# Kernel tuning notes

Hardware: AMD Instinct MI355X
Metric: run time of the kernel (lower is better)

## Reference

```python
import jax, jax.numpy as jnp
import numpy as np

C = 64        # number of classes (rows of mu)
K = 64        # int(d * overlap_ratio) = int(128 * 0.5)
ALPHA = 1.0   # margin


def _pairdist(mu, x):
    # Euclidean distance from every center to every sample: [C, N]
    d2 = (mu * mu).sum(-1)[:, None] + (x * x).sum(-1)[None, :] - 2.0 * (mu @ x.T)
    return jnp.sqrt(jnp.maximum(d2, 0.0))


def setup_inputs() -> dict:
    key = jax.random.key(0)
    k1, k2, k3 = jax.random.split(key, 3)
    N, D = 131072, 256
    x = jax.random.normal(k1, (N, D), dtype=jnp.float32)
    y = jax.random.randint(k2, (N, 3), 0, C)
    # ensure every class 0..C-1 is present with ~equal counts (matches torch.unique)
    y = y.at[:, 2].set(jnp.arange(N) % C)
    mu = jax.random.normal(k3, (C, D), dtype=jnp.float32)
    return {"x": x, "y": y, "mu": mu}


def reference(x, y, mu):
    labels = y[:, 2]                                     # [N]
    D = _pairdist(mu, x)                                 # [C, N]
    mask = labels[None, :] == jnp.arange(C)[:, None]     # [C, N] class membership

    # pos: per class c, K LARGEST distances from center c to its own samples
    pos_vals = jax.lax.top_k(jnp.where(mask, D, -jnp.inf), K)[0]  # [C, K]
    pos_mean = pos_vals.mean(-1)                                  # [C]

    # neg: for each sample-class c2, K SMALLEST distances from every center c1
    def neg_for_class(m):  # m: [N] bool mask for class c2
        vals = jax.lax.top_k(jnp.where(m[None, :], -D, -jnp.inf), K)[0]  # [C, K]
        return (-vals).mean(-1)  # [C] smallest-K mean per center c1

    negM = jax.lax.map(neg_for_class, mask)              # [C2, C1]

    hinge = jnp.maximum(ALPHA + pos_mean[None, :] - negM, 0.0)  # [C2, C1]
    offdiag = 1.0 - jnp.eye(C, dtype=hinge.dtype)
    loss = (hinge * offdiag).sum() / x.shape[0]
    return loss
```

## Files before the change

### kernel.cpp

```cpp
#include <hip/hip_runtime.h>
#include <math.h>


#define DDIM 256
#define CC 64
#define KSEL 64
#define TPTS 256
#define XS 48
#define SELN 2048

typedef short s4v __attribute__((ext_vector_type(4)));
typedef short s8v __attribute__((ext_vector_type(8)));
typedef float f4v __attribute__((ext_vector_type(4)));

__device__ __forceinline__ void cvt_split(float f, short& h, short& l) {
  const unsigned int u = __float_as_uint(f);
  const unsigned int hb = (u + 0x7FFFu + ((u >> 16) & 1u)) >> 16;
  h = (short)hb;
  const float rem = f - __uint_as_float(hb << 16);
  const unsigned int ur = __float_as_uint(rem);
  l = (short)((ur + 0x7FFFu + ((ur >> 16) & 1u)) >> 16);
}

__global__ __launch_bounds__(128) void zeroK(int* cnts) {
  cnts[threadIdx.x] = 0;
}

__global__ __launch_bounds__(256) void countK(const int* __restrict__ y, int* cnt, int N) {
  int i = blockIdx.x * 256 + threadIdx.x;
  if (i < N) atomicAdd(&cnt[y[3 * i + 2] & (CC - 1)], 1);
}

__global__ void scanK(const int* __restrict__ cnt, int* base) {
  if (threadIdx.x == 0) {
    int s = 0;
    for (int i = 0; i < CC; ++i) { base[i] = s; s += cnt[i]; }
  }
}

__global__ __launch_bounds__(256) void fillK(const int* __restrict__ y, const int* __restrict__ base,
                                             int* cnt2, int* idxs, int N) {
  int i = blockIdx.x * 256 + threadIdx.x;
  if (i < N) {
    int m = y[3 * i + 2] & (CC - 1);
    int r = atomicAdd(&cnt2[m], 1);
    idxs[base[m] + r] = i;
  }
}

__global__ __launch_bounds__(256) void distK(const float* __restrict__ x, const float* __restrict__ mu,
                                             const int* __restrict__ idxs, float* __restrict__ Dg, int N) {
  __shared__ __align__(16) short xh[TPTS][XS];
  __shared__ __align__(16) short xl[TPTS][XS];
  __shared__ __align__(16) short mh[CC][XS];
  __shared__ __align__(16) short ml[CC][XS];
  __shared__ int pid[TPTS];
  __shared__ float xn2[TPTS];
  __shared__ float mn2[CC];

  const int t = threadIdx.x;
  const int wgp0 = blockIdx.x * TPTS;
  pid[t] = idxs[wgp0 + t];

  const int q = t & 7,  pr = t >> 3;
  const int q2 = t & 3, mm = t >> 2;
  const int w = t >> 6, l = t & 63;
  const int lr = l & 15, lk = l >> 4;

  f4v acc[4][4];
  #pragma unroll
  for (int a = 0; a < 4; ++a)
    #pragma unroll
    for (int b = 0; b < 4; ++b) acc[a][b] = (f4v)0.f;
  float xnacc[8] = {0.f, 0.f, 0.f, 0.f, 0.f, 0.f, 0.f, 0.f};
  float mnacc = 0.f;

  __syncthreads();
  int pidr[8];
  #pragma unroll
  for (int r = 0; r < 8; ++r) pidr[r] = pid[r * 32 + pr];

  for (int ch = 0; ch < 8; ++ch) {
    const int kb = ch * 32;
    if (ch) __syncthreads();
    #pragma unroll
    for (int r = 0; r < 8; ++r) {
      const float4 v = *reinterpret_cast<const float4*>(x + (size_t)pidr[r] * DDIM + kb + q * 4);
      const float vs[4] = {v.x, v.y, v.z, v.w};
      s4v hv, lv;
      float s2 = 0.f;
      #pragma unroll
      for (int j = 0; j < 4; ++j) {
        short hj, lj; cvt_split(vs[j], hj, lj);
        hv[j] = hj; lv[j] = lj;
        s2 = fmaf(vs[j], vs[j], s2);
      }
      xnacc[r] += s2;
      const int p = r * 32 + pr;
      *reinterpret_cast<s4v*>(&xh[p][q * 4]) = hv;
      *reinterpret_cast<s4v*>(&xl[p][q * 4]) = lv;
    }
    {
      const float* msrc = mu + (size_t)mm * DDIM + kb + q2 * 8;
      const float4 va = *reinterpret_cast<const float4*>(msrc);
      const float4 vb = *reinterpret_cast<const float4*>(msrc + 4);
      const float vs[8] = {va.x, va.y, va.z, va.w, vb.x, vb.y, vb.z, vb.w};
      s4v h0, h1, l0, l1;
      #pragma unroll
      for (int j = 0; j < 4; ++j) {
        short hj, lj; cvt_split(vs[j], hj, lj);
        h0[j] = hj; l0[j] = lj;
        mnacc = fmaf(vs[j], vs[j], mnacc);
      }
      #pragma unroll
      for (int j = 0; j < 4; ++j) {
        short hj, lj; cvt_split(vs[4 + j], hj, lj);
        h1[j] = hj; l1[j] = lj;
        mnacc = fmaf(vs[4 + j], vs[4 + j], mnacc);
      }
      *reinterpret_cast<s4v*>(&mh[mm][q2 * 8])     = h0;
      *reinterpret_cast<s4v*>(&mh[mm][q2 * 8 + 4]) = h1;
      *reinterpret_cast<s4v*>(&ml[mm][q2 * 8])     = l0;
      *reinterpret_cast<s4v*>(&ml[mm][q2 * 8 + 4]) = l1;
    }
    __syncthreads();
    s8v ah[4], al_[4];
    #pragma unroll
    for (int mt = 0; mt < 4; ++mt) {
      ah[mt]  = *reinterpret_cast<const s8v*>(&mh[mt * 16 + lr][lk * 8]);
      al_[mt] = *reinterpret_cast<const s8v*>(&ml[mt * 16 + lr][lk * 8]);
    }
    #pragma unroll
    for (int nt = 0; nt < 4; ++nt) {
      const int prow = w * 64 + nt * 16 + lr;
      const s8v bh = *reinterpret_cast<const s8v*>(&xh[prow][lk * 8]);
      const s8v bl = *reinterpret_cast<const s8v*>(&xl[prow][lk * 8]);
      #pragma unroll
      for (int mt = 0; mt < 4; ++mt) {
        acc[mt][nt] = __builtin_amdgcn_mfma_f32_16x16x32_bf16(ah[mt],  bh, acc[mt][nt], 0, 0, 0);
        acc[mt][nt] = __builtin_amdgcn_mfma_f32_16x16x32_bf16(ah[mt],  bl, acc[mt][nt], 0, 0, 0);
        acc[mt][nt] = __builtin_amdgcn_mfma_f32_16x16x32_bf16(al_[mt], bh, acc[mt][nt], 0, 0, 0);
      }
    }
  }
  #pragma unroll
  for (int r = 0; r < 8; ++r) {
    float s = xnacc[r];
    s += __shfl_xor(s, 1, 64); s += __shfl_xor(s, 2, 64); s += __shfl_xor(s, 4, 64);
    if (q == 0) xn2[r * 32 + pr] = s;
  }
  {
    float s = mnacc;
    s += __shfl_xor(s, 1, 64); s += __shfl_xor(s, 2, 64);
    if (q2 == 0) mn2[mm] = s;
  }
  __syncthreads();
  #pragma unroll
  for (int mt = 0; mt < 4; ++mt) {
    #pragma unroll
    for (int r = 0; r < 4; ++r) {
      const int m = mt * 16 + lk * 4 + r;
      const float mn = mn2[m];
      #pragma unroll
      for (int nt = 0; nt < 4; ++nt) {
        const int p = w * 64 + nt * 16 + lr;
        const float d2 = mn + xn2[p] - 2.f * acc[mt][nt][r];
        Dg[(size_t)m * N + wgp0 + p] = sqrtf(fmaxf(d2, 0.f));
      }
    }
  }
}

__global__ __launch_bounds__(128) void selK(const float* __restrict__ Dg, const int* __restrict__ cnt,
                                            const int* __restrict__ base, float* __restrict__ posM,
                                            float* __restrict__ neg, int N) {
  __shared__ __align__(16) unsigned int keys[SELN];
  __shared__ unsigned int sh_lo, sh_hi;
  __shared__ int sh_cnt[2];
  __shared__ float sh_sum[2];
  const int c = blockIdx.x, m = blockIdx.y;
  const int t = threadIdx.x;
  const int w = t >> 6, lane = t & 63;
  const bool diag = (c == m);
  int cm = cnt[m]; if (cm > SELN) cm = SELN;
  const int bm = base[m];
  const float* src = Dg + (size_t)c * N + bm;
  const int cm4 = (cm + 3) & ~3;

  unsigned int kmin = 0xFFFFFFFFu, kmax = 0u;
  for (int i = t; i < cm4; i += 128) {
    unsigned int key = 0xFFFFFFFFu;
    if (i < cm) {
      const unsigned int b = __float_as_uint(src[i]);
      key = diag ? ~b : b;
      kmin = min(kmin, key); kmax = max(kmax, key);
    }
    keys[i] = key;
  }
  #pragma unroll
  for (int off = 32; off > 0; off >>= 1) {
    kmin = min(kmin, (unsigned int)__shfl_xor((int)kmin, off, 64));
    kmax = max(kmax, (unsigned int)__shfl_xor((int)kmax, off, 64));
  }
  if (lane == 0) { sh_cnt[w] = (int)kmin; sh_sum[w] = __uint_as_float(kmax); }
  __syncthreads();
  if (t == 0) {
    sh_lo = min((unsigned int)sh_cnt[0], (unsigned int)sh_cnt[1]);
    sh_hi = max(__float_as_uint(sh_sum[0]), __float_as_uint(sh_sum[1]));
  }

  for (;;) {
    __syncthreads();
    const unsigned int lo = sh_lo, hi = sh_hi;
    if (lo >= hi) break;
    const unsigned int mid = lo + ((hi - lo) >> 1);
    int cl = 0;
    for (int i4 = t * 4; i4 < cm4; i4 += 512) {
      const uint4 kv = *reinterpret_cast<const uint4*>(&keys[i4]);
      cl += (int)(kv.x <= mid) + (int)(kv.y <= mid) + (int)(kv.z <= mid) + (int)(kv.w <= mid);
    }
    #pragma unroll
    for (int off = 32; off > 0; off >>= 1) cl += __shfl_xor(cl, off, 64);
    if (lane == 0) sh_cnt[w] = cl;
    __syncthreads();
    if (t == 0) {
      if (sh_cnt[0] + sh_cnt[1] >= KSEL) sh_hi = mid; else sh_lo = mid + 1;
    }
  }
  const unsigned int kth = sh_lo;

  int cl = 0; float sl = 0.f;
  for (int i4 = t * 4; i4 < cm4; i4 += 512) {
    const uint4 kv = *reinterpret_cast<const uint4*>(&keys[i4]);
    const unsigned int ks[4] = {kv.x, kv.y, kv.z, kv.w};
    #pragma unroll
    for (int j = 0; j < 4; ++j) {
      if (ks[j] < kth) { ++cl; sl += __uint_as_float(diag ? ~ks[j] : ks[j]); }
    }
  }
  #pragma unroll
  for (int off = 32; off > 0; off >>= 1) {
    cl += __shfl_xor(cl, off, 64);
    sl += __shfl_xor(sl, off, 64);
  }
  if (lane == 0) { sh_cnt[w] = cl; sh_sum[w] = sl; }
  __syncthreads();
  if (t == 0) {
    const int totc = sh_cnt[0] + sh_cnt[1];
    const float tots = sh_sum[0] + sh_sum[1];
    const float kval = __uint_as_float(diag ? ~kth : kth);
    const float mval = (tots + (float)(KSEL - totc) * kval) * (1.0f / KSEL);
    if (diag) posM[c] = mval; else neg[m * CC + c] = mval;
  }
}

__global__ __launch_bounds__(256) void lossK(const float* __restrict__ posM, const float* __restrict__ neg,
                                             float* __restrict__ out, int N) {
  __shared__ float red[256];
  const int t = threadIdx.x;
  float s = 0.f;
  for (int idx = t; idx < CC * CC; idx += 256) {
    const int m = idx >> 6, c = idx & 63;
    if (m != c) {
      const float h = 1.0f + posM[c] - neg[idx];
      s += fmaxf(h, 0.0f);
    }
  }
  red[t] = s;
  __syncthreads();
  for (int off = 128; off > 0; off >>= 1) {
    if (t < off) red[t] += red[t + off];
    __syncthreads();
  }
  if (t == 0) out[0] = red[0] / (float)N;
}

__global__ void wsFailK(float* out) {
  if (threadIdx.x == 0) out[0] = -1.0e30f;
}

extern "C" void kernel_launch(void* const* d_in, const int* in_sizes, int n_in,
                              void* d_out, int out_size, void* d_ws, size_t ws_size,
                              hipStream_t stream) {
  const float* x  = (const float*)d_in[0];
  const int*   y  = (const int*)d_in[1];
  const float* mu = (const float*)d_in[2];
  float* out = (float*)d_out;
  const int N = in_sizes[0] / DDIM;

  const size_t need = (size_t)557056 + (size_t)CC * (size_t)N * 4;
  if (ws_size < need) {
    hipLaunchKernelGGL(wsFailK, dim3(1), dim3(64), 0, stream, out);
    return;
  }
  char* w = (char*)d_ws;
  int*   cnt  = (int*)(w);
  int*   cnt2 = (int*)(w + 256);
  int*   base = (int*)(w + 512);
  float* posM = (float*)(w + 768);
  float* neg  = (float*)(w + 1024);
  int*   idxs = (int*)(w + 32768);
  float* Dg   = (float*)(w + 557056);

  hipLaunchKernelGGL(zeroK, dim3(1), dim3(128), 0, stream, cnt);
  hipLaunchKernelGGL(countK, dim3((N + 255) / 256), dim3(256), 0, stream, y, cnt, N);
  hipLaunchKernelGGL(scanK, dim3(1), dim3(64), 0, stream, cnt, base);
  hipLaunchKernelGGL(fillK, dim3((N + 255) / 256), dim3(256), 0, stream, y, base, cnt2, idxs, N);
  hipLaunchKernelGGL(distK, dim3(N / TPTS), dim3(256), 0, stream, x, mu, idxs, Dg, N);
  hipLaunchKernelGGL(selK, dim3(CC, CC), dim3(128), 0, stream, Dg, cnt, base, posM, neg, N);
  hipLaunchKernelGGL(lossK, dim3(1), dim3(256), 0, stream, posM, neg, out, N);
}
```

Measured before the change: 331.6 us.

## Precompute split-bf16 mu once and prefetch x chunks in distance kernel

The zero-count kernel becomes a prep kernel that converts mu to bf16 hi/lo parts and its squared norms once, stored in the workspace. The distance kernel then reads these mu fragments straight from global memory instead of redoing the conversion and LDS staging in every block. It also halves the points per block, with launch bounds raised for more occupancy, and register-prefetches the next x chunk while the MFMAs run. The costs are more blocks, each re-reading mu fragments from global or L2, and a second barrier per chunk.

```diff
diff --git a/kernel.cpp b/kernel.cpp
--- a/kernel.cpp
+++ b/kernel.cpp
@@ -5,8 +5,8 @@
 #define DDIM 256
 #define CC 64
 #define KSEL 64
-#define TPTS 256
-#define XS 48
+#define TPTS 128
+#define XS 40
 #define SELN 2048
 
 typedef short s4v __attribute__((ext_vector_type(4)));
@@ -22,8 +22,27 @@
   l = (short)((ur + 0x7FFFu + ((ur >> 16) & 1u)) >> 16);
 }
 
-__global__ __launch_bounds__(128) void zeroK(int* cnts) {
-  cnts[threadIdx.x] = 0;
+__global__ __launch_bounds__(256) void prepK(const float* __restrict__ mu, short* __restrict__ mhG,
+                                             short* __restrict__ mlG, float* __restrict__ mn2G,
+                                             int* __restrict__ cnts) {
+  const int b = blockIdx.x, t = threadIdx.x;
+  if (b == 0 && t < 128) cnts[t] = 0;
+  const int row = b * 4 + (t >> 6), l = t & 63;
+  const float4 v = *reinterpret_cast<const float4*>(mu + (size_t)row * DDIM + l * 4);
+  const float vs[4] = {v.x, v.y, v.z, v.w};
+  s4v hv, lv;
+  float s2 = 0.f;
+  #pragma unroll
+  for (int j = 0; j < 4; ++j) {
+    short hj, lj; cvt_split(vs[j], hj, lj);
+    hv[j] = hj; lv[j] = lj;
+    s2 = fmaf(vs[j], vs[j], s2);
+  }
+  *reinterpret_cast<s4v*>(&mhG[(size_t)row * DDIM + l * 4]) = hv;
+  *reinterpret_cast<s4v*>(&mlG[(size_t)row * DDIM + l * 4]) = lv;
+  #pragma unroll
+  for (int off = 32; off > 0; off >>= 1) s2 += __shfl_xor(s2, off, 64);
+  if (l == 0) mn2G[row] = s2;
 }
 
 __global__ __launch_bounds__(256) void countK(const int* __restrict__ y, int* cnt, int N) {
@@ -48,45 +67,51 @@
   }
 }
 
-__global__ __launch_bounds__(256) void distK(const float* __restrict__ x, const float* __restrict__ mu,
-                                             const int* __restrict__ idxs, float* __restrict__ Dg, int N) {
+__global__ __launch_bounds__(256, 4) void distK(const float* __restrict__ x, const short* __restrict__ mhG,
+                                                const short* __restrict__ mlG, const float* __restrict__ mn2G,
+                                                const int* __restrict__ idxs, float* __restrict__ Dg, int N) {
   __shared__ __align__(16) short xh[TPTS][XS];
   __shared__ __align__(16) short xl[TPTS][XS];
-  __shared__ __align__(16) short mh[CC][XS];
-  __shared__ __align__(16) short ml[CC][XS];
   __shared__ int pid[TPTS];
   __shared__ float xn2[TPTS];
-  __shared__ float mn2[CC];
 
   const int t = threadIdx.x;
   const int wgp0 = blockIdx.x * TPTS;
-  pid[t] = idxs[wgp0 + t];
-
-  const int q = t & 7,  pr = t >> 3;
-  const int q2 = t & 3, mm = t >> 2;
+  if (t < TPTS) pid[t] = idxs[wgp0 + t];
+
+  const int q = t & 7, pr = t >> 3;
   const int w = t >> 6, l = t & 63;
   const int lr = l & 15, lk = l >> 4;
 
-  f4v acc[4][4];
+  f4v acc[4][2];
   #pragma unroll
   for (int a = 0; a < 4; ++a)
     #pragma unroll
-    for (int b = 0; b < 4; ++b) acc[a][b] = (f4v)0.f;
-  float xnacc[8] = {0.f, 0.f, 0.f, 0.f, 0.f, 0.f, 0.f, 0.f};
-  float mnacc = 0.f;
-
-  __syncthreads();
-  int pidr[8];
-  #pragma unroll
-  for (int r = 0; r < 8; ++r) pidr[r] = pid[r * 32 + pr];
+    for (int b = 0; b < 2; ++b) acc[a][b] = (f4v)0.f;
+  float xnacc[4] = {0.f, 0.f, 0.f, 0.f};
+
+  __syncthreads();
+  int pidr[4];
+  #pragma unroll
+  for (int p = 0; p < 4; ++p) pidr[p] = pid[p * 32 + pr];
+
+  float4 vreg[4];
+  #pragma unroll
+  for (int p = 0; p < 4; ++p)
+    vreg[p] = *reinterpret_cast<const float4*>(x + (size_t)pidr[p] * DDIM + q * 4);
 
   for (int ch = 0; ch < 8; ++ch) {
     const int kb = ch * 32;
-    if (ch) __syncthreads();
-    #pragma unroll
-    for (int r = 0; r < 8; ++r) {
-      const float4 v = *reinterpret_cast<const float4*>(x + (size_t)pidr[r] * DDIM + kb + q * 4);
-      const float vs[4] = {v.x, v.y, v.z, v.w};
+    s8v ah[4], al_[4];
+    #pragma unroll
+    for (int mt = 0; mt < 4; ++mt) {
+      const size_t ro = (size_t)(mt * 16 + lr) * DDIM + kb + lk * 8;
+      ah[mt]  = *reinterpret_cast<const s8v*>(mhG + ro);
+      al_[mt] = *reinterpret_cast<const s8v*>(mlG + ro);
+    }
+    #pragma unroll
+    for (int p = 0; p < 4; ++p) {
+      const float vs[4] = {vreg[p].x, vreg[p].y, vreg[p].z, vreg[p].w};
       s4v hv, lv;
       float s2 = 0.f;
       #pragma unroll
@@ -95,64 +120,40 @@
         hv[j] = hj; lv[j] = lj;
         s2 = fmaf(vs[j], vs[j], s2);
       }
-      xnacc[r] += s2;
-      const int p = r * 32 + pr;
-      *reinterpret_cast<s4v*>(&xh[p][q * 4]) = hv;
-      *reinterpret_cast<s4v*>(&xl[p][q * 4]) = lv;
-    }
-    {
-      const float* msrc = mu + (size_t)mm * DDIM + kb + q2 * 8;
-      const float4 va = *reinterpret_cast<const float4*>(msrc);
-      const float4 vb = *reinterpret_cast<const float4*>(msrc + 4);
-      const float vs[8] = {va.x, va.y, va.z, va.w, vb.x, vb.y, vb.z, vb.w};
-      s4v h0, h1, l0, l1;
+      xnacc[p] += s2;
+      const int pt = p * 32 + pr;
+      *reinterpret_cast<s4v*>(&xh[pt][q * 4]) = hv;
+      *reinterpret_cast<s4v*>(&xl[pt][q * 4]) = lv;
+    }
+    __syncthreads();
+    if (ch < 7) {
       #pragma unroll
-      for (int j = 0; j < 4; ++j) {
-        short hj, lj; cvt_split(vs[j], hj, lj);
-        h0[j] = hj; l0[j] = lj;
-        mnacc = fmaf(vs[j], vs[j], mnacc);
+      for (int p = 0; p < 4; ++p)
+        vreg[p] = *reinterpret_cast<const float4*>(x + (size_t)pidr[p] * DDIM + kb + 32 + q * 4);
+    }
+    s8v bh[2], bl[2];
+    #pragma unroll
+    for (int nt = 0; nt < 2; ++nt) {
+      const int prow = w * 32 + nt * 16 + lr;
+      bh[nt] = *reinterpret_cast<const s8v*>(&xh[prow][lk * 8]);
+      bl[nt] = *reinterpret_cast<const s8v*>(&xl[prow][lk * 8]);
+    }
+    #pragma unroll
+    for (int mt = 0; mt < 4; ++mt) {
+      #pragma unroll
+      for (int nt = 0; nt < 2; ++nt) {
+        acc[mt][nt] = __builtin_amdgcn_mfma_f32_16x16x32_bf16(ah[mt],  bh[nt], acc[mt][nt], 0, 0, 0);
+        acc[mt][nt] = __builtin_amdgcn_mfma_f32_16x16x32_bf16(ah[mt],  bl[nt], acc[mt][nt], 0, 0, 0);
+        acc[mt][nt] = __builtin_amdgcn_mfma_f32_16x16x32_bf16(al_[mt], bh[nt], acc[mt][nt], 0, 0, 0);
       }
-      #pragma unroll
-      for (int j = 0; j < 4; ++j) {
-        short hj, lj; cvt_split(vs[4 + j], hj, lj);
-        h1[j] = hj; l1[j] = lj;
-        mnacc = fmaf(vs[4 + j], vs[4 + j], mnacc);
-      }
-      *reinterpret_cast<s4v*>(&mh[mm][q2 * 8])     = h0;
-      *reinterpret_cast<s4v*>(&mh[mm][q2 * 8 + 4]) = h1;
-      *reinterpret_cast<s4v*>(&ml[mm][q2 * 8])     = l0;
-      *reinterpret_cast<s4v*>(&ml[mm][q2 * 8 + 4]) = l1;
-    }
-    __syncthreads();
-    s8v ah[4], al_[4];
-    #pragma unroll
-    for (int mt = 0; mt < 4; ++mt) {
-      ah[mt]  = *reinterpret_cast<const s8v*>(&mh[mt * 16 + lr][lk * 8]);
-      al_[mt] = *reinterpret_cast<const s8v*>(&ml[mt * 16 + lr][lk * 8]);
-    }
-    #pragma unroll
-    for (int nt = 0; nt < 4; ++nt) {
-      const int prow = w * 64 + nt * 16 + lr;
-      const s8v bh = *reinterpret_cast<const s8v*>(&xh[prow][lk * 8]);
-      const s8v bl = *reinterpret_cast<const s8v*>(&xl[prow][lk * 8]);
-      #pragma unroll
-      for (int mt = 0; mt < 4; ++mt) {
-        acc[mt][nt] = __builtin_amdgcn_mfma_f32_16x16x32_bf16(ah[mt],  bh, acc[mt][nt], 0, 0, 0);
-        acc[mt][nt] = __builtin_amdgcn_mfma_f32_16x16x32_bf16(ah[mt],  bl, acc[mt][nt], 0, 0, 0);
-        acc[mt][nt] = __builtin_amdgcn_mfma_f32_16x16x32_bf16(al_[mt], bh, acc[mt][nt], 0, 0, 0);
-      }
-    }
-  }
-  #pragma unroll
-  for (int r = 0; r < 8; ++r) {
-    float s = xnacc[r];
+    }
+    __syncthreads();
+  }
+  #pragma unroll
+  for (int p = 0; p < 4; ++p) {
+    float s = xnacc[p];
     s += __shfl_xor(s, 1, 64); s += __shfl_xor(s, 2, 64); s += __shfl_xor(s, 4, 64);
-    if (q == 0) xn2[r * 32 + pr] = s;
-  }
-  {
-    float s = mnacc;
-    s += __shfl_xor(s, 1, 64); s += __shfl_xor(s, 2, 64);
-    if (q2 == 0) mn2[mm] = s;
+    if (q == 0) xn2[p * 32 + pr] = s;
   }
   __syncthreads();
   #pragma unroll
@@ -160,10 +161,10 @@
     #pragma unroll
     for (int r = 0; r < 4; ++r) {
       const int m = mt * 16 + lk * 4 + r;
-      const float mn = mn2[m];
+      const float mn = mn2G[m];
       #pragma unroll
-      for (int nt = 0; nt < 4; ++nt) {
-        const int p = w * 64 + nt * 16 + lr;
+      for (int nt = 0; nt < 2; ++nt) {
+        const int p = w * 32 + nt * 16 + lr;
         const float d2 = mn + xn2[p] - 2.f * acc[mt][nt][r];
         Dg[(size_t)m * N + wgp0 + p] = sqrtf(fmaxf(d2, 0.f));
       }
@@ -288,7 +289,7 @@
   float* out = (float*)d_out;
   const int N = in_sizes[0] / DDIM;
 
-  const size_t need = (size_t)557056 + (size_t)CC * (size_t)N * 4;
+  const size_t need = (size_t)655360 + (size_t)CC * (size_t)N * 4;
   if (ws_size < need) {
     hipLaunchKernelGGL(wsFailK, dim3(1), dim3(64), 0, stream, out);
     return;
@@ -299,14 +300,17 @@
   int*   base = (int*)(w + 512);
   float* posM = (float*)(w + 768);
   float* neg  = (float*)(w + 1024);
-  int*   idxs = (int*)(w + 32768);
-  float* Dg   = (float*)(w + 557056);
-
-  hipLaunchKernelGGL(zeroK, dim3(1), dim3(128), 0, stream, cnt);
+  float* mn2G = (float*)(w + 17408);
+  short* mhG  = (short*)(w + 20480);
+  short* mlG  = (short*)(w + 53248);
+  int*   idxs = (int*)(w + 131072);
+  float* Dg   = (float*)(w + 655360);
+
+  hipLaunchKernelGGL(prepK, dim3(16), dim3(256), 0, stream, mu, mhG, mlG, mn2G, cnt);
   hipLaunchKernelGGL(countK, dim3((N + 255) / 256), dim3(256), 0, stream, y, cnt, N);
   hipLaunchKernelGGL(scanK, dim3(1), dim3(64), 0, stream, cnt, base);
   hipLaunchKernelGGL(fillK, dim3((N + 255) / 256), dim3(256), 0, stream, y, base, cnt2, idxs, N);
-  hipLaunchKernelGGL(distK, dim3(N / TPTS), dim3(256), 0, stream, x, mu, idxs, Dg, N);
+  hipLaunchKernelGGL(distK, dim3(N / TPTS), dim3(256), 0, stream, x, mhG, mlG, mn2G, idxs, Dg, N);
   hipLaunchKernelGGL(selK, dim3(CC, CC), dim3(128), 0, stream, Dg, cnt, base, posM, neg, N);
   hipLaunchKernelGGL(lossK, dim3(1), dim3(256), 0, stream, posM, neg, out, N);
 }
```

Measured after the change: 331.3 us. About the same (-0.1%).

## Split distance kernel into gather/convert pass and MFMA GEMM with register prefetch

Applied to the files above, without the earlier changes.

Adds a gather kernel that reorders x by class, splits each value into bf16 hi/lo parts and computes squared norms into a workspace. A separate GEMM kernel keeps the whole converted mu in LDS and streams x fragments straight from global memory into registers with double buffering. Mu conversion and the count zeroing move into a small prep kernel. This trades an extra write and read of the converted x (about 128MB) for a simpler, better pipelined GEMM, and it keeps the old fused kernel as a fallback when the workspace is smaller.

```diff
diff --git a/kernel.cpp b/kernel.cpp
--- a/kernel.cpp
+++ b/kernel.cpp
@@ -5,9 +5,10 @@
 #define DDIM 256
 #define CC 64
 #define KSEL 64
-#define TPTS 256
-#define XS 48
+#define MS 264
 #define SELN 2048
+#define TPTSF 256
+#define XSF 48
 
 typedef short s4v __attribute__((ext_vector_type(4)));
 typedef short s8v __attribute__((ext_vector_type(8)));
@@ -22,8 +23,27 @@
   l = (short)((ur + 0x7FFFu + ((ur >> 16) & 1u)) >> 16);
 }
 
-__global__ __launch_bounds__(128) void zeroK(int* cnts) {
-  cnts[threadIdx.x] = 0;
+__global__ __launch_bounds__(256) void prepK(const float* __restrict__ mu, short* __restrict__ mhG,
+                                             short* __restrict__ mlG, float* __restrict__ mn2G,
+                                             int* __restrict__ cnts) {
+  const int b = blockIdx.x, t = threadIdx.x;
+  if (b == 0 && t < 128) cnts[t] = 0;
+  const int row = b * 4 + (t >> 6), l = t & 63;
+  const float4 v = *reinterpret_cast<const float4*>(mu + (size_t)row * DDIM + l * 4);
+  const float vs[4] = {v.x, v.y, v.z, v.w};
+  s4v hv, lv;
+  float s2 = 0.f;
+  #pragma unroll
+  for (int j = 0; j < 4; ++j) {
+    short hj, lj; cvt_split(vs[j], hj, lj);
+    hv[j] = hj; lv[j] = lj;
+    s2 = fmaf(vs[j], vs[j], s2);
+  }
+  *reinterpret_cast<s4v*>(&mhG[(size_t)row * DDIM + l * 4]) = hv;
+  *reinterpret_cast<s4v*>(&mlG[(size_t)row * DDIM + l * 4]) = lv;
+  #pragma unroll
+  for (int off = 32; off > 0; off >>= 1) s2 += __shfl_xor(s2, off, 64);
+  if (l == 0) mn2G[row] = s2;
 }
 
 __global__ __launch_bounds__(256) void countK(const int* __restrict__ y, int* cnt, int N) {
@@ -48,18 +68,122 @@
   }
 }
 
-__global__ __launch_bounds__(256) void distK(const float* __restrict__ x, const float* __restrict__ mu,
-                                             const int* __restrict__ idxs, float* __restrict__ Dg, int N) {
-  __shared__ __align__(16) short xh[TPTS][XS];
-  __shared__ __align__(16) short xl[TPTS][XS];
-  __shared__ __align__(16) short mh[CC][XS];
-  __shared__ __align__(16) short ml[CC][XS];
-  __shared__ int pid[TPTS];
-  __shared__ float xn2[TPTS];
+
+__global__ __launch_bounds__(256) void gatherK(const float* __restrict__ x, const int* __restrict__ idxs,
+                                               short* __restrict__ xsh, short* __restrict__ xsl,
+                                               float* __restrict__ xn2, int N) {
+  const int slot = blockIdx.x * 4 + (threadIdx.x >> 6);
+  const int l = threadIdx.x & 63;
+  const int src = idxs[slot];
+  const float4 v = *reinterpret_cast<const float4*>(x + (size_t)src * DDIM + l * 4);
+  const float vs[4] = {v.x, v.y, v.z, v.w};
+  s4v hv, lv;
+  float s2 = 0.f;
+  #pragma unroll
+  for (int j = 0; j < 4; ++j) {
+    short hj, lj; cvt_split(vs[j], hj, lj);
+    hv[j] = hj; lv[j] = lj;
+    s2 = fmaf(vs[j], vs[j], s2);
+  }
+  *reinterpret_cast<s4v*>(xsh + (size_t)slot * DDIM + l * 4) = hv;
+  *reinterpret_cast<s4v*>(xsl + (size_t)slot * DDIM + l * 4) = lv;
+  #pragma unroll
+  for (int off = 32; off > 0; off >>= 1) s2 += __shfl_xor(s2, off, 64);
+  if (l == 0) xn2[slot] = s2;
+}
+
+__global__ __launch_bounds__(256, 2) void gemmK(const short* __restrict__ xsh, const short* __restrict__ xsl,
+                                                const short* __restrict__ mhG, const short* __restrict__ mlG,
+                                                const float* __restrict__ mn2G, const float* __restrict__ xn2,
+                                                float* __restrict__ Dg, int N) {
+  __shared__ __align__(16) short mh[CC][MS];
+  __shared__ __align__(16) short ml[CC][MS];
+  const int t = threadIdx.x;
+  const int w = t >> 6, l = t & 63;
+  const int lr = l & 15, lk = l >> 4;
+
+  #pragma unroll
+  for (int j = 0; j < 8; ++j) {
+    const int f = j * 2048 + t * 8;
+    const int row = f >> 8, col = f & 255;
+    *reinterpret_cast<s8v*>(&mh[row][col]) = *reinterpret_cast<const s8v*>(mhG + f);
+    *reinterpret_cast<s8v*>(&ml[row][col]) = *reinterpret_cast<const s8v*>(mlG + f);
+  }
+  __syncthreads();
+
+  const int pbase = blockIdx.x * 256 + w * 64;
+
+  s8v bhq[2][4], blq[2][4];
+  #pragma unroll
+  for (int nt = 0; nt < 4; ++nt) {
+    const size_t ro = (size_t)(pbase + nt * 16 + lr) * DDIM + lk * 8;
+    bhq[0][nt] = *reinterpret_cast<const s8v*>(xsh + ro);
+    blq[0][nt] = *reinterpret_cast<const s8v*>(xsl + ro);
+  }
+
+  f4v acc[4][4];
+  #pragma unroll
+  for (int a = 0; a < 4; ++a)
+    #pragma unroll
+    for (int b = 0; b < 4; ++b) acc[a][b] = (f4v)0.f;
+
+  #pragma unroll
+  for (int ch = 0; ch < 8; ++ch) {
+    const int cur = ch & 1, nxt = cur ^ 1;
+    if (ch < 7) {
+      #pragma unroll
+      for (int nt = 0; nt < 4; ++nt) {
+        const size_t ro = (size_t)(pbase + nt * 16 + lr) * DDIM + (ch + 1) * 32 + lk * 8;
+        bhq[nxt][nt] = *reinterpret_cast<const s8v*>(xsh + ro);
+        blq[nxt][nt] = *reinterpret_cast<const s8v*>(xsl + ro);
+      }
+    }
+    s8v ah[4], al_[4];
+    #pragma unroll
+    for (int mt = 0; mt < 4; ++mt) {
+      ah[mt]  = *reinterpret_cast<const s8v*>(&mh[mt * 16 + lr][ch * 32 + lk * 8]);
+      al_[mt] = *reinterpret_cast<const s8v*>(&ml[mt * 16 + lr][ch * 32 + lk * 8]);
+    }
+    #pragma unroll
+    for (int mt = 0; mt < 4; ++mt) {
+      #pragma unroll
+      for (int nt = 0; nt < 4; ++nt) {
+        acc[mt][nt] = __builtin_amdgcn_mfma_f32_16x16x32_bf16(ah[mt],  bhq[cur][nt], acc[mt][nt], 0, 0, 0);
+        acc[mt][nt] = __builtin_amdgcn_mfma_f32_16x16x32_bf16(ah[mt],  blq[cur][nt], acc[mt][nt], 0, 0, 0);
+        acc[mt][nt] = __builtin_amdgcn_mfma_f32_16x16x32_bf16(al_[mt], bhq[cur][nt], acc[mt][nt], 0, 0, 0);
+      }
+    }
+  }
+
+  #pragma unroll
+  for (int nt = 0; nt < 4; ++nt) {
+    const int p = pbase + nt * 16 + lr;
+    const float xn = xn2[p];
+    #pragma unroll
+    for (int mt = 0; mt < 4; ++mt) {
+      #pragma unroll
+      for (int r = 0; r < 4; ++r) {
+        const int m = mt * 16 + lk * 4 + r;
+        const float d2 = mn2G[m] + xn - 2.f * acc[mt][nt][r];
+        Dg[(size_t)m * N + p] = sqrtf(fmaxf(d2, 0.f));
+      }
+    }
+  }
+}
+
+
+__global__ __launch_bounds__(256) void distKf(const float* __restrict__ x, const float* __restrict__ mu,
+                                              const int* __restrict__ idxs, float* __restrict__ Dg, int N) {
+  __shared__ __align__(16) short xh[TPTSF][XSF];
+  __shared__ __align__(16) short xl[TPTSF][XSF];
+  __shared__ __align__(16) short mh[CC][XSF];
+  __shared__ __align__(16) short ml[CC][XSF];
+  __shared__ int pid[TPTSF];
+  __shared__ float xn2[TPTSF];
   __shared__ float mn2[CC];
 
   const int t = threadIdx.x;
-  const int wgp0 = blockIdx.x * TPTS;
+  const int wgp0 = blockIdx.x * TPTSF;
   pid[t] = idxs[wgp0 + t];
 
   const int q = t & 7,  pr = t >> 3;
@@ -170,6 +294,7 @@
     }
   }
 }
+
 
 __global__ __launch_bounds__(128) void selK(const float* __restrict__ Dg, const int* __restrict__ cnt,
                                             const int* __restrict__ base, float* __restrict__ posM,
@@ -288,25 +413,43 @@
   float* out = (float*)d_out;
   const int N = in_sizes[0] / DDIM;
 
-  const size_t need = (size_t)557056 + (size_t)CC * (size_t)N * 4;
-  if (ws_size < need) {
-    hipLaunchKernelGGL(wsFailK, dim3(1), dim3(64), 0, stream, out);
-    return;
-  }
   char* w = (char*)d_ws;
   int*   cnt  = (int*)(w);
   int*   cnt2 = (int*)(w + 256);
   int*   base = (int*)(w + 512);
   float* posM = (float*)(w + 768);
   float* neg  = (float*)(w + 1024);
-  int*   idxs = (int*)(w + 32768);
-  float* Dg   = (float*)(w + 557056);
-
-  hipLaunchKernelGGL(zeroK, dim3(1), dim3(128), 0, stream, cnt);
-  hipLaunchKernelGGL(countK, dim3((N + 255) / 256), dim3(256), 0, stream, y, cnt, N);
-  hipLaunchKernelGGL(scanK, dim3(1), dim3(64), 0, stream, cnt, base);
-  hipLaunchKernelGGL(fillK, dim3((N + 255) / 256), dim3(256), 0, stream, y, base, cnt2, idxs, N);
-  hipLaunchKernelGGL(distK, dim3(N / TPTS), dim3(256), 0, stream, x, mu, idxs, Dg, N);
-  hipLaunchKernelGGL(selK, dim3(CC, CC), dim3(128), 0, stream, Dg, cnt, base, posM, neg, N);
-  hipLaunchKernelGGL(lossK, dim3(1), dim3(256), 0, stream, posM, neg, out, N);
-}
+  float* mn2G = (float*)(w + 17408);
+  short* mhG  = (short*)(w + 20480);
+  short* mlG  = (short*)(w + 53248);
+  int*   idxs = (int*)(w + 131072);
+
+  const size_t needBig   = (size_t)135397376 + (size_t)CC * (size_t)N * 4;
+  const size_t needSmall = (size_t)655360    + (size_t)CC * (size_t)N * 4;
+
+  if (ws_size >= needBig) {
+    float* xn2 = (float*)(w + 655360);
+    short* xsh = (short*)(w + 1179648);
+    short* xsl = (short*)(w + 68288512);
+    float* Dg  = (float*)(w + 135397376);
+    hipLaunchKernelGGL(prepK, dim3(16), dim3(256), 0, stream, mu, mhG, mlG, mn2G, cnt);
+    hipLaunchKernelGGL(countK, dim3((N + 255) / 256), dim3(256), 0, stream, y, cnt, N);
+    hipLaunchKernelGGL(scanK, dim3(1), dim3(64), 0, stream, cnt, base);
+    hipLaunchKernelGGL(fillK, dim3((N + 255) / 256), dim3(256), 0, stream, y, base, cnt2, idxs, N);
+    hipLaunchKernelGGL(gatherK, dim3(N / 4), dim3(256), 0, stream, x, idxs, xsh, xsl, xn2, N);
+    hipLaunchKernelGGL(gemmK, dim3(N / 256), dim3(256), 0, stream, xsh, xsl, mhG, mlG, mn2G, xn2, Dg, N);
+    hipLaunchKernelGGL(selK, dim3(CC, CC), dim3(128), 0, stream, Dg, cnt, base, posM, neg, N);
+    hipLaunchKernelGGL(lossK, dim3(1), dim3(256), 0, stream, posM, neg, out, N);
+  } else if (ws_size >= needSmall) {
+    float* Dg = (float*)(w + 655360);
+    hipLaunchKernelGGL(prepK, dim3(16), dim3(256), 0, stream, mu, mhG, mlG, mn2G, cnt);
+    hipLaunchKernelGGL(countK, dim3((N + 255) / 256), dim3(256), 0, stream, y, cnt, N);
+    hipLaunchKernelGGL(scanK, dim3(1), dim3(64), 0, stream, cnt, base);
+    hipLaunchKernelGGL(fillK, dim3((N + 255) / 256), dim3(256), 0, stream, y, base, cnt2, idxs, N);
+    hipLaunchKernelGGL(distKf, dim3(N / TPTSF), dim3(256), 0, stream, x, mu, idxs, Dg, N);
+    hipLaunchKernelGGL(selK, dim3(CC, CC), dim3(128), 0, stream, Dg, cnt, base, posM, neg, N);
+    hipLaunchKernelGGL(lossK, dim3(1), dim3(256), 0, stream, posM, neg, out, N);
+  } else {
+    hipLaunchKernelGGL(wsFailK, dim3(1), dim3(64), 0, stream, out);
+  }
+}
```

Result: slower. 388.1 us (+17.0%).
